# Kernel optimization log

Measured on AMD Instinct MI355X. Metric: run time of the kernel, lower is better.

The kernel has to match this reference:

```python
import jax, jax.numpy as jnp
import numpy as np

THETA = 10000.0
NUM_HEADS = 16


def _rope_tables(seq_len, d_k, dtype):
    exponent = jnp.arange(d_k // 2, dtype=jnp.float32) * (2.0 / d_k)
    inv_freq = THETA ** (-exponent)                      # (d_k/2,)
    pos = jnp.arange(seq_len, dtype=jnp.float32)
    angles = pos[:, None] * inv_freq[None, :]            # (n, d_k/2)
    return jnp.cos(angles).astype(dtype), jnp.sin(angles).astype(dtype)


def _apply_rope(x, cos, sin):
    # x: (..., n, d_k); interleaved pair convention: pairs are (x[...,2i], x[...,2i+1])
    x1 = x[..., 0::2]
    x2 = x[..., 1::2]
    r1 = x1 * cos - x2 * sin
    r2 = x1 * sin + x2 * cos
    return jnp.stack([r1, r2], axis=-1).reshape(x.shape)


def setup_inputs() -> dict:
    key = jax.random.key(0)
    ks = jax.random.split(key, 5)
    B, N, D = 2, 4096, 1024
    std = (2.0 / (D + D)) ** 0.5
    return {
        "x": jax.random.normal(ks[0], (B, N, D), dtype=jnp.float32),
        "Wq": jax.random.normal(ks[1], (D, D), dtype=jnp.float32) * std,
        "Wk": jax.random.normal(ks[2], (D, D), dtype=jnp.float32) * std,
        "Wv": jax.random.normal(ks[3], (D, D), dtype=jnp.float32) * std,
        "Wo": jax.random.normal(ks[4], (D, D), dtype=jnp.float32) * std,
    }


def reference(x, Wq, Wk, Wv, Wo):
    B, N, D = x.shape
    H = NUM_HEADS
    d_k = D // H

    def proj(W):
        y = jnp.einsum('oi,bni->bno', W, x)
        return y.reshape(B, N, H, d_k).transpose(0, 2, 1, 3)  # (b,h,n,d)

    Q, K, V = proj(Wq), proj(Wk), proj(Wv)

    cos, sin = _rope_tables(N, d_k, x.dtype)
    Q = _apply_rope(Q, cos, sin)
    K = _apply_rope(K, cos, sin)

    scores = jnp.einsum('bhnd,bhmd->bhnm', Q, K) / jnp.sqrt(jnp.asarray(d_k, x.dtype))
    causal = jnp.tril(jnp.ones((N, N), dtype=bool))
    scores = jnp.where(causal, scores, -jnp.inf)
    attn = jax.nn.softmax(scores, axis=-1)
    out = jnp.einsum('bhnm,bhmd->bhnd', attn, V)          # (b,h,n,d)
    out = out.transpose(0, 2, 1, 3).reshape(B, N, D)
    return jnp.einsum('oi,bni->bno', Wo, out)
```

## Files before the change

### kernel.cpp

```cpp
#include <hip/hip_runtime.h>
#include <hip/hip_bf16.h>
#include <stdint.h>

typedef __attribute__((ext_vector_type(8))) short short8;
typedef __attribute__((ext_vector_type(4))) float f32x4;
typedef __attribute__((ext_vector_type(2))) unsigned uint32x2;

#define NSEQ 4096
#define DMODEL 1024
#define MROWS 8192

__device__ __forceinline__ unsigned short f2bf(float f) {
  union { float f; unsigned u; } v; v.f = f;
  unsigned r = v.u + 0x7fffu + ((v.u >> 16) & 1u);
  return (unsigned short)(r >> 16);
}

__device__ __forceinline__ unsigned pkc(float lo, float hi) {
  unsigned r;
  asm("v_cvt_pk_bf16_f32 %0, %1, %2" : "=v"(r) : "v"(lo), "v"(hi));
  return r;
}

__device__ __forceinline__ void gload16(const unsigned short* g, unsigned short* l) {
  __builtin_amdgcn_global_load_lds(
      (const __attribute__((address_space(1))) unsigned int*)g,
      (__attribute__((address_space(3))) unsigned int*)l, 16, 0, 0);
}

__device__ __forceinline__ void pexch(unsigned x, unsigned y, unsigned& w_lo, unsigned& w_hi) {
  uint32x2 t = __builtin_amdgcn_permlane32_swap(x, y, false, false);
  uint32x2 u = __builtin_amdgcn_permlane16_swap(t[0], t[1], false, false);
  w_lo = u[0];
  w_hi = u[1];
}

__global__ void k_prep(const float* __restrict__ x,
                       const float* __restrict__ Wq, const float* __restrict__ Wk,
                       const float* __restrict__ Wv, const float* __restrict__ Wo,
                       unsigned short* __restrict__ xb, unsigned short* __restrict__ Wb,
                       float* __restrict__ cosT, float* __restrict__ sinT) {
  int bid = blockIdx.x;
  if (bid < 8192) {
    int i = (bid * 256 + threadIdx.x) * 4;
    float4 v = *(const float4*)(x + i);
    ushort4 o;
    o.x = f2bf(v.x); o.y = f2bf(v.y); o.z = f2bf(v.z); o.w = f2bf(v.w);
    *(ushort4*)(xb + i) = o;
  } else if (bid < 12288) {
    int r = bid - 8192;
    int z = r >> 10;
    const float* src = (z == 0) ? Wq : (z == 1) ? Wk : (z == 2) ? Wv : Wo;
    float sc = (z == 0) ? 0.18033688011112042f : 1.0f;
    int i = ((r & 1023) * 256 + threadIdx.x) * 4;
    float4 v = *(const float4*)(src + i);
    ushort4 o;
    o.x = f2bf(v.x * sc); o.y = f2bf(v.y * sc); o.z = f2bf(v.z * sc); o.w = f2bf(v.w * sc);
    *(ushort4*)(Wb + (size_t)z * 1048576 + i) = o;
  } else {
    int i = (bid - 12288) * 256 + threadIdx.x;
    int pos = i >> 5, j = i & 31;
    float invf = exp2f(-(float)j * 0.41524101186092029f);
    float ang = (float)pos * invf;
    cosT[i] = cosf(ang);
    sinT[i] = sinf(ang);
  }
}

__global__ __launch_bounds__(256, 2) void k_gemm_qkv(
    const unsigned short* __restrict__ A,
    const unsigned short* __restrict__ Bw,
    unsigned short* __restrict__ obf,
    unsigned short* __restrict__ Vt,
    const float* __restrict__ cosT, const float* __restrict__ sinT) {
  const int wg = (blockIdx.x & 7) * 64 + (blockIdx.x >> 3);
  const int bn = wg & 7, bm = wg >> 3;
  const int t = threadIdx.x;
  const int w = t >> 6, lane = t & 63;
  const int wr = w >> 1, wc = w & 1;
  const int lr = lane & 15, lg = lane >> 4;

  __shared__ __align__(16) unsigned short SM[4][128 * 64];

  const unsigned short* Ab = A + (size_t)bm * 128 * DMODEL;
  const unsigned short* Bb = Bw + (size_t)bn * 128 * DMODEL;
  const int trow = t >> 3, tcol = (t & 7) * 8;

  f32x4 acc[3][4][4] = {};

  for (int k0 = 0; k0 < DMODEL; k0 += 64) {
#pragma unroll
    for (int c = 0; c < 4; ++c) {
      gload16(Ab + (size_t)(c * 32 + trow) * DMODEL + k0 + tcol, &SM[0][c * 2048 + t * 8]);
#pragma unroll
      for (int z = 0; z < 3; ++z)
        gload16(Bb + (size_t)z * 1048576 + (size_t)(c * 32 + trow) * DMODEL + k0 + tcol,
                &SM[1 + z][c * 2048 + t * 8]);
    }
    asm volatile("s_waitcnt vmcnt(0)" ::: "memory");
    __syncthreads();
#pragma unroll
    for (int kk = 0; kk < 2; ++kk) {
      short8 af[4];
#pragma unroll
      for (int mi = 0; mi < 4; ++mi)
        af[mi] = *(const short8*)&SM[0][(wr * 64 + mi * 16 + lr) * 64 + kk * 32 + lg * 8];
#pragma unroll
      for (int z = 0; z < 3; ++z) {
        short8 bfr[4];
#pragma unroll
        for (int ni = 0; ni < 4; ++ni)
          bfr[ni] = *(const short8*)&SM[1 + z][(wc * 64 + ni * 16 + lr) * 64 + kk * 32 + lg * 8];
#pragma unroll
        for (int mi = 0; mi < 4; ++mi)
#pragma unroll
          for (int ni = 0; ni < 4; ++ni)
            acc[z][mi][ni] = __builtin_amdgcn_mfma_f32_16x16x32_bf16(af[mi], bfr[ni], acc[z][mi][ni], 0, 0, 0);
      }
    }
    __syncthreads();
  }

  float* Cf = (float*)&SM[0][0];
#pragma unroll
  for (int z = 0; z < 2; ++z) {
    unsigned short* oz = obf + (size_t)z * MROWS * DMODEL;
#pragma unroll
    for (int half = 0; half < 2; ++half) {
      __syncthreads();
      if (wr == half) {
#pragma unroll
        for (int mi = 0; mi < 4; ++mi)
#pragma unroll
          for (int ni = 0; ni < 4; ++ni)
#pragma unroll
            for (int r = 0; r < 4; ++r) {
              int row = mi * 16 + lg * 4 + r;
              int col = (wc * 64 + ni * 16 + lr) ^ (lg << 3);
              Cf[row * 128 + col] = acc[z][mi][ni][r];
            }
      }
      __syncthreads();
      int pr = t >> 2;
      int gm = bm * 128 + half * 64 + pr;
      int pos = gm & (NSEQ - 1);
      int xorv = ((pr >> 2) & 3) << 3;
      const float* cB = cosT + pos * 32;
      const float* sB = sinT + pos * 32;
      unsigned short* orow = oz + (size_t)gm * DMODEL + bn * 128;
#pragma unroll
      for (int k = 0; k < 4; ++k) {
        int c0 = (t & 3) * 8 + k * 32;
        int cs = c0 ^ xorv;
        float4 va = *(const float4*)&Cf[pr * 128 + cs];
        float4 vb = *(const float4*)&Cf[pr * 128 + cs + 4];
        int j0 = (c0 & 63) >> 1;
        float4 cv = *(const float4*)&cB[j0];
        float4 sv = *(const float4*)&sB[j0];
        uint4 o;
        o.x = pkc(va.x * cv.x - va.y * sv.x, va.x * sv.x + va.y * cv.x);
        o.y = pkc(va.z * cv.y - va.w * sv.y, va.z * sv.y + va.w * cv.y);
        o.z = pkc(vb.x * cv.z - vb.y * sv.z, vb.x * sv.z + vb.y * cv.z);
        o.w = pkc(vb.z * cv.w - vb.w * sv.w, vb.z * sv.w + vb.w * cv.w);
        *(uint4*)(orow + c0) = o;
      }
    }
  }
#pragma unroll
  for (int mi = 0; mi < 4; ++mi)
#pragma unroll
    for (int ni = 0; ni < 4; ++ni) {
      int gm0 = bm * 128 + wr * 64 + mi * 16 + lg * 4;
      int gn = bn * 128 + wc * 64 + ni * 16 + lr;
      int b = gm0 >> 12, n = gm0 & (NSEQ - 1);
      int h = gn >> 6, d = gn & 63;
      uint2 u;
      u.x = pkc(acc[2][mi][ni][0], acc[2][mi][ni][1]);
      u.y = pkc(acc[2][mi][ni][2], acc[2][mi][ni][3]);
      *(uint2*)(Vt + ((size_t)((b * 16 + h) * 64 + d)) * NSEQ + n) = u;
    }
}

__global__ __launch_bounds__(256) void k_gemm_bt(
    const unsigned short* __restrict__ A,
    const unsigned short* __restrict__ Bw,
    float* __restrict__ of32,
    int K) {
  const int N = DMODEL;
  const int q8 = gridDim.x >> 3;
  const int wg = (blockIdx.x & 7) * q8 + (blockIdx.x >> 3);
  const int rr = wg & 511;
  const int bn = rr & 7, bm = rr >> 3;

  const int t = threadIdx.x;
  const int w = t >> 6, lane = t & 63;
  const int wr = w >> 1, wc = w & 1;
  const int lr = lane & 15, lg = lane >> 4;

  __shared__ __align__(16) unsigned short SM[2][128 * 64];
  unsigned short* Al = SM[0];
  unsigned short* Bl = SM[1];

  const unsigned short* Ab = A + (size_t)bm * 128 * K;
  const unsigned short* Bb = Bw + (size_t)bn * 128 * K;
  const int trow = t >> 3, tcol = (t & 7) * 8;

  f32x4 acc[4][4] = {};

  for (int k0 = 0; k0 < K; k0 += 64) {
#pragma unroll
    for (int c = 0; c < 4; ++c) {
      gload16(Ab + (size_t)(c * 32 + trow) * K + k0 + tcol, &Al[c * 2048 + t * 8]);
      gload16(Bb + (size_t)(c * 32 + trow) * K + k0 + tcol, &Bl[c * 2048 + t * 8]);
    }
    asm volatile("s_waitcnt vmcnt(0)" ::: "memory");
    __syncthreads();
#pragma unroll
    for (int kk = 0; kk < 2; ++kk) {
      short8 af[4], bfr[4];
#pragma unroll
      for (int mi = 0; mi < 4; ++mi)
        af[mi] = *(const short8*)&Al[(wr * 64 + mi * 16 + lr) * 64 + kk * 32 + lg * 8];
#pragma unroll
      for (int ni = 0; ni < 4; ++ni)
        bfr[ni] = *(const short8*)&Bl[(wc * 64 + ni * 16 + lr) * 64 + kk * 32 + lg * 8];
#pragma unroll
      for (int mi = 0; mi < 4; ++mi)
#pragma unroll
        for (int ni = 0; ni < 4; ++ni)
          acc[mi][ni] = __builtin_amdgcn_mfma_f32_16x16x32_bf16(af[mi], bfr[ni], acc[mi][ni], 0, 0, 0);
    }
    __syncthreads();
  }

  float* Cf = (float*)&SM[0][0];
#pragma unroll
  for (int half = 0; half < 2; ++half) {
    if (half) __syncthreads();
    if (wr == half) {
#pragma unroll
      for (int mi = 0; mi < 4; ++mi)
#pragma unroll
        for (int ni = 0; ni < 4; ++ni)
#pragma unroll
          for (int r = 0; r < 4; ++r) {
            int row = mi * 16 + lg * 4 + r;
            int col = (wc * 64 + ni * 16 + lr) ^ (lg << 3);
            Cf[row * 128 + col] = acc[mi][ni][r];
          }
    }
    __syncthreads();
    int pr = t >> 2;
    int gm = bm * 128 + half * 64 + pr;
    int xorv = ((pr >> 2) & 3) << 3;
    float* orow = of32 + (size_t)gm * N + bn * 128;
#pragma unroll
    for (int k = 0; k < 4; ++k) {
      int c0 = (t & 3) * 8 + k * 32;
      int cs = c0 ^ xorv;
      float4 va = *(const float4*)&Cf[pr * 128 + cs];
      float4 vb = *(const float4*)&Cf[pr * 128 + cs + 4];
      *(float4*)(orow + c0) = va;
      *(float4*)(orow + c0 + 4) = vb;
    }
  }
}

__global__ __launch_bounds__(256, 2) void k_attn12(
    const unsigned short* __restrict__ Qb,
    const unsigned short* __restrict__ Kb,
    const unsigned short* __restrict__ Vtg,
    unsigned short* __restrict__ AO) {
  const int id = blockIdx.x;
  const int bh = id & 31;
  const int pq = id >> 5;
  const int b = bh >> 4, h = bh & 15;
  const int t = threadIdx.x;
  const int w = t >> 6, lane = t & 63;
  const int lr = lane & 15, hi4 = lane >> 4;
  const size_t rowbase = (size_t)b * NSEQ;

  __shared__ __align__(16) unsigned short Kl[2][64 * 64];
  __shared__ __align__(16) unsigned short Vl[2][64 * 64];
  __shared__ __align__(16) unsigned short Pl[4][16 * 64];

  const int pswz = (lr & 7) << 3;

  short8 ones;
#pragma unroll
  for (int i = 0; i < 8; ++i) ones[i] = (short)0x3F80;

#define STAGE(buf, kv0)                                                                   \
  {                                                                                       \
    _Pragma("unroll")                                                                     \
    for (int it = 0; it < 2; ++it) {                                                      \
      int c = t + it * 256;                                                               \
      int row = c >> 3, sg = (c & 7) ^ (row & 7);                                         \
      gload16(Kb + (rowbase + (kv0) + row) * DMODEL + h * 64 + sg * 8, &Kl[buf][c * 8]);  \
      gload16(Vtg + ((size_t)bh * 64 + row) * NSEQ + (kv0) + sg * 8, &Vl[buf][c * 8]);    \
    }                                                                                     \
  }

#pragma unroll
  for (int qi = 0; qi < 2; ++qi) {
    const int qt = qi ? pq : (31 - pq);
    const int q0w = qt * 128 + w * 32;

    short8 qf[2][2];
#pragma unroll
    for (int sub = 0; sub < 2; ++sub) {
      const unsigned short* qp = Qb + (rowbase + q0w + sub * 16 + lr) * DMODEL + h * 64 + hi4 * 8;
#pragma unroll
      for (int s = 0; s < 2; ++s)
        qf[sub][s] = *(const short8*)(qp + s * 32);
    }

    f32x4 oacc[2][4] = {};
    f32x4 lacc[2] = {};
    const int nkv = (qt + 1) * 2;

    STAGE(0, 0);
    asm volatile("s_waitcnt vmcnt(0)" ::: "memory");
    __syncthreads();

    for (int ib = 0; ib < nkv; ++ib) {
      const int kv0 = ib * 64, cur = ib & 1;
      if (ib + 1 < nkv) STAGE(cur ^ 1, kv0 + 64);

      if (kv0 <= q0w + 31) {
        short8 Kf[4][2], Vf[2][4];
#pragma unroll
        for (int t4 = 0; t4 < 4; ++t4)
#pragma unroll
          for (int s = 0; s < 2; ++s)
            Kf[t4][s] = *(const short8*)&Kl[cur][(t4 * 16 + lr) * 64 + (((s * 4 + hi4) ^ (lr & 7)) * 8)];
#pragma unroll
        for (int c = 0; c < 2; ++c)
#pragma unroll
          for (int dt = 0; dt < 4; ++dt)
            Vf[c][dt] = *(const short8*)&Vl[cur][(dt * 16 + lr) * 64 + (((c * 4 + hi4) ^ (lr & 7)) * 8)];

#pragma unroll
        for (int sub = 0; sub < 2; ++sub) {
          const int qs = q0w + sub * 16;
          const int qlane = qs + lr;
          f32x4 sa[4];
          const f32x4 zz = {0.f, 0.f, 0.f, 0.f};
          __builtin_amdgcn_s_setprio(1);
#pragma unroll
          for (int t4 = 0; t4 < 4; ++t4) {
            f32x4 x = __builtin_amdgcn_mfma_f32_16x16x32_bf16(Kf[t4][0], qf[sub][0], zz, 0, 0, 0);
            sa[t4] = __builtin_amdgcn_mfma_f32_16x16x32_bf16(Kf[t4][1], qf[sub][1], x, 0, 0, 0);
          }
          __builtin_amdgcn_s_setprio(0);
          if (kv0 + 63 > qs) {
#pragma unroll
            for (int t4 = 0; t4 < 4; ++t4)
#pragma unroll
              for (int r = 0; r < 4; ++r)
                if (kv0 + t4 * 16 + hi4 * 4 + r > qlane) sa[t4][r] = -1e30f;
          }
#pragma unroll
          for (int t4 = 0; t4 < 4; ++t4)
#pragma unroll
            for (int r = 0; r < 4; ++r)
              sa[t4][r] = __builtin_amdgcn_exp2f(sa[t4][r]);

          unsigned a0 = pkc(sa[0][0], sa[0][1]), a1 = pkc(sa[0][2], sa[0][3]);
          unsigned a2 = pkc(sa[1][0], sa[1][1]), a3 = pkc(sa[1][2], sa[1][3]);
          unsigned a4 = pkc(sa[2][0], sa[2][1]), a5 = pkc(sa[2][2], sa[2][3]);
          unsigned a6 = pkc(sa[3][0], sa[3][1]), a7 = pkc(sa[3][2], sa[3][3]);
          unsigned w0, w1, w2, w3, x0, x1, x2, x3;
          pexch(a0, a2, w0, w2);
          pexch(a1, a3, w1, w3);
          pexch(a4, a6, x0, x2);
          pexch(a5, a7, x1, x3);
          union { uint4 u; short8 s; } P0, P1;
          P0.u.x = w0; P0.u.y = w1; P0.u.z = w2; P0.u.w = w3;
          P1.u.x = x0; P1.u.y = x1; P1.u.z = x2; P1.u.w = x3;
          short8 pf0 = P0.s;
          short8 pf1 = P1.s;

          __builtin_amdgcn_s_setprio(1);
#pragma unroll
          for (int dt = 0; dt < 4; ++dt) {
            oacc[sub][dt] = __builtin_amdgcn_mfma_f32_16x16x32_bf16(Vf[0][dt], pf0, oacc[sub][dt], 0, 0, 0);
            oacc[sub][dt] = __builtin_amdgcn_mfma_f32_16x16x32_bf16(Vf[1][dt], pf1, oacc[sub][dt], 0, 0, 0);
          }
          lacc[sub] = __builtin_amdgcn_mfma_f32_16x16x32_bf16(ones, pf0, lacc[sub], 0, 0, 0);
          lacc[sub] = __builtin_amdgcn_mfma_f32_16x16x32_bf16(ones, pf1, lacc[sub], 0, 0, 0);
          __builtin_amdgcn_s_setprio(0);
        }
      }
      asm volatile("s_waitcnt vmcnt(0)" ::: "memory");
      __syncthreads();
    }

#pragma unroll
    for (int sub = 0; sub < 2; ++sub) {
      float inv = 1.f / lacc[sub][0];
#pragma unroll
      for (int dt = 0; dt < 4; ++dt) {
        uint2 u;
        u.x = pkc(oacc[sub][dt][0] * inv, oacc[sub][dt][1] * inv);
        u.y = pkc(oacc[sub][dt][2] * inv, oacc[sub][dt][3] * inv);
        *(uint2*)&Pl[w][lr * 64 + ((dt * 16 + hi4 * 4) ^ pswz)] = u;
      }
      asm volatile("s_waitcnt lgkmcnt(0)" ::: "memory");
      __builtin_amdgcn_sched_barrier(0);
      int q2 = lane >> 2, ch = (lane & 3) * 16;
      int qswz = (q2 & 7) << 3;
      uint4 r0 = *(const uint4*)&Pl[w][q2 * 64 + (ch ^ qswz)];
      uint4 r1 = *(const uint4*)&Pl[w][q2 * 64 + ((ch + 8) ^ qswz)];
      unsigned short* op = AO + (rowbase + q0w + sub * 16 + q2) * DMODEL + h * 64 + ch;
      *(uint4*)op = r0;
      *(uint4*)(op + 8) = r1;
      __syncthreads();
    }
  }
}

extern "C" void kernel_launch(void* const* d_in, const int* in_sizes, int n_in,
                              void* d_out, int out_size, void* d_ws, size_t ws_size,
                              hipStream_t stream) {
  const float* x  = (const float*)d_in[0];
  const float* Wq = (const float*)d_in[1];
  const float* Wk = (const float*)d_in[2];
  const float* Wv = (const float*)d_in[3];
  const float* Wo = (const float*)d_in[4];
  float* out = (float*)d_out;
  char* ws = (char*)d_ws;

  unsigned short* xb  = (unsigned short*)(ws);
  unsigned short* Wb  = (unsigned short*)(ws + 16777216);
  unsigned short* Qb  = (unsigned short*)(ws + 25165824);
  unsigned short* Kb  = Qb + 8388608;
  unsigned short* Vtg = (unsigned short*)(ws + 58720256);
  unsigned short* AO  = (unsigned short*)(ws + 75497472);
  float* cosT = (float*)(ws + 92274688);
  float* sinT = (float*)(ws + 92798976);

  k_prep<<<12800, 256, 0, stream>>>(x, Wq, Wk, Wv, Wo, xb, Wb, cosT, sinT);

  k_gemm_qkv<<<512, 256, 0, stream>>>(xb, Wb, Qb, Vtg, cosT, sinT);

  k_attn12<<<512, 256, 0, stream>>>(Qb, Kb, Vtg, AO);

  k_gemm_bt<<<512, 256, 0, stream>>>(AO, Wb + 3145728, out, DMODEL);
}
```

Before: 191.1 us.

## Process both causal q-tiles in one shared K/V pass in attention

The attention kernel now keeps accumulators for both paired query tiles and iterates once over the K/V range of the larger tile. Each K/V block is staged into LDS and loaded into fragments once, then applied to both tiles where the causal mask allows. This removes the redundant global loads and LDS reads for the shared prefix. In exchange it doubles the accumulator and Q fragment registers, which may reduce occupancy or cause spills.

After: 189.2 us. No clear change (-1.0%).

```diff
diff --git a/kernel.cpp b/kernel.cpp
--- a/kernel.cpp
+++ b/kernel.cpp
@@ -266,7 +266,7 @@
   }
 }
 
-__global__ __launch_bounds__(256, 2) void k_attn12(
+__global__ __launch_bounds__(256, 2) void k_attn15(
     const unsigned short* __restrict__ Qb,
     const unsigned short* __restrict__ Kb,
     const unsigned short* __restrict__ Vtg,
@@ -301,45 +301,49 @@
     }                                                                                     \
   }
 
-#pragma unroll
-  for (int qi = 0; qi < 2; ++qi) {
-    const int qt = qi ? pq : (31 - pq);
-    const int q0w = qt * 128 + w * 32;
-
-    short8 qf[2][2];
+  int q0t[2];
+  q0t[0] = (31 - pq) * 128 + w * 32;
+  q0t[1] = pq * 128 + w * 32;
+
+  short8 qf[2][2][2];
+#pragma unroll
+  for (int tt = 0; tt < 2; ++tt)
 #pragma unroll
     for (int sub = 0; sub < 2; ++sub) {
-      const unsigned short* qp = Qb + (rowbase + q0w + sub * 16 + lr) * DMODEL + h * 64 + hi4 * 8;
+      const unsigned short* qp = Qb + (rowbase + q0t[tt] + sub * 16 + lr) * DMODEL + h * 64 + hi4 * 8;
 #pragma unroll
       for (int s = 0; s < 2; ++s)
-        qf[sub][s] = *(const short8*)(qp + s * 32);
-    }
-
-    f32x4 oacc[2][4] = {};
-    f32x4 lacc[2] = {};
-    const int nkv = (qt + 1) * 2;
-
-    STAGE(0, 0);
-    asm volatile("s_waitcnt vmcnt(0)" ::: "memory");
-    __syncthreads();
-
-    for (int ib = 0; ib < nkv; ++ib) {
-      const int kv0 = ib * 64, cur = ib & 1;
-      if (ib + 1 < nkv) STAGE(cur ^ 1, kv0 + 64);
-
+        qf[tt][sub][s] = *(const short8*)(qp + s * 32);
+    }
+
+  f32x4 oacc[2][2][4] = {};
+  f32x4 lacc[2][2] = {};
+  const int nkv = (32 - pq) * 2;
+
+  STAGE(0, 0);
+  asm volatile("s_waitcnt vmcnt(0)" ::: "memory");
+  __syncthreads();
+
+  for (int ib = 0; ib < nkv; ++ib) {
+    const int kv0 = ib * 64, cur = ib & 1;
+    if (ib + 1 < nkv) STAGE(cur ^ 1, kv0 + 64);
+
+    short8 Kf[4][2], Vf[2][4];
+#pragma unroll
+    for (int t4 = 0; t4 < 4; ++t4)
+#pragma unroll
+      for (int s = 0; s < 2; ++s)
+        Kf[t4][s] = *(const short8*)&Kl[cur][(t4 * 16 + lr) * 64 + (((s * 4 + hi4) ^ (lr & 7)) * 8)];
+#pragma unroll
+    for (int c = 0; c < 2; ++c)
+#pragma unroll
+      for (int dt = 0; dt < 4; ++dt)
+        Vf[c][dt] = *(const short8*)&Vl[cur][(dt * 16 + lr) * 64 + (((c * 4 + hi4) ^ (lr & 7)) * 8)];
+
+#pragma unroll
+    for (int tt = 0; tt < 2; ++tt) {
+      const int q0w = q0t[tt];
       if (kv0 <= q0w + 31) {
-        short8 Kf[4][2], Vf[2][4];
-#pragma unroll
-        for (int t4 = 0; t4 < 4; ++t4)
-#pragma unroll
-          for (int s = 0; s < 2; ++s)
-            Kf[t4][s] = *(const short8*)&Kl[cur][(t4 * 16 + lr) * 64 + (((s * 4 + hi4) ^ (lr & 7)) * 8)];
-#pragma unroll
-        for (int c = 0; c < 2; ++c)
-#pragma unroll
-          for (int dt = 0; dt < 4; ++dt)
-            Vf[c][dt] = *(const short8*)&Vl[cur][(dt * 16 + lr) * 64 + (((c * 4 + hi4) ^ (lr & 7)) * 8)];
-
 #pragma unroll
         for (int sub = 0; sub < 2; ++sub) {
           const int qs = q0w + sub * 16;
@@ -349,8 +353,8 @@
           __builtin_amdgcn_s_setprio(1);
 #pragma unroll
           for (int t4 = 0; t4 < 4; ++t4) {
-            f32x4 x = __builtin_amdgcn_mfma_f32_16x16x32_bf16(Kf[t4][0], qf[sub][0], zz, 0, 0, 0);
-            sa[t4] = __builtin_amdgcn_mfma_f32_16x16x32_bf16(Kf[t4][1], qf[sub][1], x, 0, 0, 0);
+            f32x4 x = __builtin_amdgcn_mfma_f32_16x16x32_bf16(Kf[t4][0], qf[tt][sub][0], zz, 0, 0, 0);
+            sa[t4] = __builtin_amdgcn_mfma_f32_16x16x32_bf16(Kf[t4][1], qf[tt][sub][1], x, 0, 0, 0);
           }
           __builtin_amdgcn_s_setprio(0);
           if (kv0 + 63 > qs) {
@@ -384,26 +388,29 @@
           __builtin_amdgcn_s_setprio(1);
 #pragma unroll
           for (int dt = 0; dt < 4; ++dt) {
-            oacc[sub][dt] = __builtin_amdgcn_mfma_f32_16x16x32_bf16(Vf[0][dt], pf0, oacc[sub][dt], 0, 0, 0);
-            oacc[sub][dt] = __builtin_amdgcn_mfma_f32_16x16x32_bf16(Vf[1][dt], pf1, oacc[sub][dt], 0, 0, 0);
+            oacc[tt][sub][dt] = __builtin_amdgcn_mfma_f32_16x16x32_bf16(Vf[0][dt], pf0, oacc[tt][sub][dt], 0, 0, 0);
+            oacc[tt][sub][dt] = __builtin_amdgcn_mfma_f32_16x16x32_bf16(Vf[1][dt], pf1, oacc[tt][sub][dt], 0, 0, 0);
           }
-          lacc[sub] = __builtin_amdgcn_mfma_f32_16x16x32_bf16(ones, pf0, lacc[sub], 0, 0, 0);
-          lacc[sub] = __builtin_amdgcn_mfma_f32_16x16x32_bf16(ones, pf1, lacc[sub], 0, 0, 0);
+          lacc[tt][sub] = __builtin_amdgcn_mfma_f32_16x16x32_bf16(ones, pf0, lacc[tt][sub], 0, 0, 0);
+          lacc[tt][sub] = __builtin_amdgcn_mfma_f32_16x16x32_bf16(ones, pf1, lacc[tt][sub], 0, 0, 0);
           __builtin_amdgcn_s_setprio(0);
         }
       }
-      asm volatile("s_waitcnt vmcnt(0)" ::: "memory");
-      __syncthreads();
-    }
-
+    }
+    asm volatile("s_waitcnt vmcnt(0)" ::: "memory");
+    __syncthreads();
+  }
+
+#pragma unroll
+  for (int tt = 0; tt < 2; ++tt)
 #pragma unroll
     for (int sub = 0; sub < 2; ++sub) {
-      float inv = 1.f / lacc[sub][0];
+      float inv = 1.f / lacc[tt][sub][0];
 #pragma unroll
       for (int dt = 0; dt < 4; ++dt) {
         uint2 u;
-        u.x = pkc(oacc[sub][dt][0] * inv, oacc[sub][dt][1] * inv);
-        u.y = pkc(oacc[sub][dt][2] * inv, oacc[sub][dt][3] * inv);
+        u.x = pkc(oacc[tt][sub][dt][0] * inv, oacc[tt][sub][dt][1] * inv);
+        u.y = pkc(oacc[tt][sub][dt][2] * inv, oacc[tt][sub][dt][3] * inv);
         *(uint2*)&Pl[w][lr * 64 + ((dt * 16 + hi4 * 4) ^ pswz)] = u;
       }
       asm volatile("s_waitcnt lgkmcnt(0)" ::: "memory");
@@ -412,12 +419,12 @@
       int qswz = (q2 & 7) << 3;
       uint4 r0 = *(const uint4*)&Pl[w][q2 * 64 + (ch ^ qswz)];
       uint4 r1 = *(const uint4*)&Pl[w][q2 * 64 + ((ch + 8) ^ qswz)];
-      unsigned short* op = AO + (rowbase + q0w + sub * 16 + q2) * DMODEL + h * 64 + ch;
+      unsigned short* op = AO + (rowbase + q0t[tt] + sub * 16 + q2) * DMODEL + h * 64 + ch;
       *(uint4*)op = r0;
       *(uint4*)(op + 8) = r1;
-      __syncthreads();
-    }
-  }
+      asm volatile("s_waitcnt lgkmcnt(0)" ::: "memory");
+      __builtin_amdgcn_sched_barrier(0);
+    }
 }
 
 extern "C" void kernel_launch(void* const* d_in, const int* in_sizes, int n_in,
@@ -444,7 +451,7 @@
 
   k_gemm_qkv<<<512, 256, 0, stream>>>(xb, Wb, Qb, Vtg, cosT, sinT);
 
-  k_attn12<<<512, 256, 0, stream>>>(Qb, Kb, Vtg, AO);
+  k_attn15<<<512, 256, 0, stream>>>(Qb, Kb, Vtg, AO);
 
   k_gemm_bt<<<512, 256, 0, stream>>>(AO, Wb + 3145728, out, DMODEL);
 }
```
